# Performance work log

Hardware: AMD Instinct MI355X
Metric: run time of the kernel (lower is better)

## Reference

```python
import jax, jax.numpy as jnp
import numpy as np

DIMS = 256


def setup_inputs() -> dict:
    key = jax.random.key(0)
    ks = jax.random.split(key, 7)
    c = DIMS
    x = jax.random.normal(ks[0], (8, c, 64, 64), dtype=jnp.float32)
    s = 1.0 / np.sqrt(c)  # conv2d default init scale ~ U(-1/sqrt(fan_in),..)
    wq = jax.random.uniform(ks[1], (c, c), jnp.float32, -s, s)
    wk = jax.random.uniform(ks[2], (c, c), jnp.float32, -s, s)
    wv = jax.random.uniform(ks[3], (c, c), jnp.float32, -s, s)
    bq = jax.random.uniform(ks[4], (c,), jnp.float32, -s, s)
    bk = jax.random.uniform(ks[5], (c,), jnp.float32, -s, s)
    bv = jax.random.uniform(ks[6], (c,), jnp.float32, -s, s)
    return {"x": x, "wq": wq, "wk": wk, "wv": wv, "bq": bq, "bk": bk, "bv": bv}


def reference(x, wq, wk, wv, bq, bk, bv):
    b, c, h, w = x.shape
    xt = x.reshape(b, c, h * w).transpose(0, 2, 1)  # (b, hw, c)
    # 1x1 conv == per-pixel linear over channels; wq has shape (out_c, in_c)
    q = xt @ wq.T + bq  # (b, hw, c)
    k = xt @ wk.T + bk
    v = xt @ wv.T + bv
    scores = jnp.einsum('bnc,bmc->bnm', q, k) / jnp.sqrt(jnp.asarray(c, x.dtype))
    attn = jax.nn.softmax(scores, axis=-1)  # (b, hw, hw)
    out = jnp.einsum('bnm,bmc->bnc', attn, v)  # (b, hw, c)
    return out.transpose(0, 2, 1).reshape(b, c, h, w)
```

## Files before the change

kernel.cpp:

```cpp
#include <hip/hip_runtime.h>

#define NB 8
#define CC 256
#define NN 4096
#define KVB 64
#define NT (NN / KVB)

typedef __attribute__((ext_vector_type(8))) __bf16 bf16x8;
typedef __attribute__((ext_vector_type(4))) float f32x4;
typedef unsigned short u16;
typedef unsigned int u32;

#define GLL(g, l) __builtin_amdgcn_global_load_lds(                         \
    (const __attribute__((address_space(1))) void*)(g),                     \
    (__attribute__((address_space(3))) void*)(l), 16, 0, 0)

static __device__ __forceinline__ u16 f2b(float f) {
  unsigned u = __float_as_uint(f);
  u += 0x7FFF + ((u >> 16) & 1);
  return (u16)(u >> 16);
}

static __device__ __forceinline__ void plswap(u32& a, u32& b) {
  asm volatile("v_permlane32_swap_b32 %0, %1" : "+v"(a), "+v"(b));
}
static __device__ __forceinline__ void plswap16(u32& a, u32& b) {
  asm volatile("v_permlane16_swap_b32 %0, %1" : "+v"(a), "+v"(b));
}

__global__ __launch_bounds__(256) void k_cvtw(const float* __restrict__ wq,
                                              const float* __restrict__ wk,
                                              const float* __restrict__ wv,
                                              u16* __restrict__ wb) {
  const int i = blockIdx.x * 256 + threadIdx.x;
  const int z = blockIdx.y;
  const float* s = z == 0 ? wq : (z == 1 ? wk : wv);
  wb[(size_t)z * CC * CC + i] = f2b(s[i]);
}

__global__ __launch_bounds__(256) void k_qkv(const float* __restrict__ x,
                                             const u16* __restrict__ wb,
                                             const float* __restrict__ bq,
                                             const float* __restrict__ bk,
                                             const float* __restrict__ bv,
                                             u16* __restrict__ Qb,
                                             u16* __restrict__ Kb,
                                             u16* __restrict__ VTb) {
  __shared__ __align__(16) u16 At[64 * 256];

  const int b = blockIdx.y, n0 = blockIdx.x * 64;
  const int tid = threadIdx.x;
  const int wid = tid >> 6, lane = tid & 63;
  const int lr = lane & 15, lq = lane >> 4;

  {
    const int ccol = (lane & 15) * 4;
#pragma unroll
    for (int i = 0; i < 16; ++i) {
      const int c = wid * 64 + i * 4 + (lane >> 4);
      const f32x4 v = *(const f32x4*)(x + ((size_t)b * CC + c) * NN + n0 + ccol);
#pragma unroll
      for (int j = 0; j < 4; ++j) {
        const int nr = ccol + j;
        *(u16*)((char*)At + nr * 512 + ((c * 2) ^ ((nr & 7) << 4))) = f2b(v[j]);
      }
    }
  }
  __syncthreads();

  const int i0 = wid * 64;
#pragma unroll
  for (int z = 0; z < 3; ++z) {
    const u16* w = wb + (size_t)z * CC * CC;
    const float* bias = z == 0 ? bq : (z == 1 ? bk : bv);
    const float sc = z == 0 ? 0.09016844136959962f : 1.0f;

    f32x4 acc[4][4];
#pragma unroll
    for (int mt = 0; mt < 4; ++mt)
#pragma unroll
      for (int it = 0; it < 4; ++it) acc[mt][it] = (f32x4){0.f, 0.f, 0.f, 0.f};

#pragma unroll
    for (int s = 0; s < 8; ++s) {
      const int kb2 = s * 64 + lq * 16;
      bf16x8 av[4], bm[4];
#pragma unroll
      for (int mt = 0; mt < 4; ++mt) {
        const int row = mt * 16 + lr;
        av[mt] = *(const bf16x8*)((const char*)At + row * 512 + (kb2 ^ ((row & 7) << 4)));
      }
#pragma unroll
      for (int it = 0; it < 4; ++it)
        bm[it] = *(const bf16x8*)(w + (size_t)(i0 + it * 16 + lr) * CC + s * 32 + lq * 8);
#pragma unroll
      for (int mt = 0; mt < 4; ++mt)
#pragma unroll
        for (int it = 0; it < 4; ++it)
          acc[mt][it] = __builtin_amdgcn_mfma_f32_16x16x32_bf16(av[mt], bm[it], acc[mt][it], 0, 0, 0);
    }

#pragma unroll
    for (int it = 0; it < 4; ++it) {
      const int i = i0 + it * 16 + lr;
      const float bb = bias[i];
#pragma unroll
      for (int mt = 0; mt < 4; ++mt) {
        f32x4 v = acc[mt][it];
        if (z == 2) {
          ushort4 p;
          p.x = f2b(v[0] + bb);
          p.y = f2b(v[1] + bb);
          p.z = f2b(v[2] + bb);
          p.w = f2b(v[3] + bb);
          *(ushort4*)(VTb + ((size_t)b * CC + i) * NN + n0 + mt * 16 + lq * 4) = p;
        } else {
          u16* O = (z == 0 ? Qb : Kb) + ((size_t)b * NN + n0 + mt * 16 + lq * 4) * CC + i;
#pragma unroll
          for (int r = 0; r < 4; ++r) O[(size_t)r * CC] = f2b((v[r] + bb) * sc);
        }
      }
    }
  }
}

__global__ __launch_bounds__(512, 2) void k_attn(const u16* __restrict__ Qb,
                                                 const u16* __restrict__ Kb,
                                                 const u16* __restrict__ VTb,
                                                 float* __restrict__ out) {
  __shared__ __align__(16) char smem[131072];
  __shared__ float l_s[2][128];

  const int bid = blockIdx.x;
  const int b = bid & 7;
  const int q0 = (bid >> 3) * 128;
  const int tid = threadIdx.x;
  const int wid = tid >> 6, lane = tid & 63;
  const int lr = lane & 15, lq = lane >> 4;
  const int kvg = wid & 1, qg = wid >> 1;

  const char* Kbase = (const char*)(Kb + (size_t)b * NN * CC);
  const char* Vbase = (const char*)(VTb + (size_t)b * CC * NN);

  const int kc0 = wid * 4;
  const int krow_off = lane >> 5;
  const int kbyt = (lane & 31) * 16;
  const int vrow_off = lane >> 3;
  const int vbyt = (lane & 7) * 16;

  auto stage = [&](int buf, int kv) {
#pragma unroll
    for (int i = 0; i < 4; ++i) {
      const int c = kc0 + i;
      const int row = c * 2 + krow_off;
      GLL(Kbase + (size_t)(kv + row) * (CC * 2) + (kbyt ^ ((row & 7) << 4)),
          smem + buf * 32768 + c * 1024);
      const int vr = c * 8 + vrow_off;
      GLL(Vbase + (size_t)vr * (NN * 2) + (size_t)kv * 2 + (vbyt ^ ((vr & 7) << 4)),
          smem + 65536 + buf * 32768 + c * 1024);
    }
  };

  bf16x8 qf[16];
  {
    const u16* Qp = Qb + ((size_t)b * NN + q0 + qg * 32 + lr) * CC + lq * 8;
#pragma unroll
    for (int qt = 0; qt < 2; ++qt)
#pragma unroll
      for (int s = 0; s < 8; ++s)
        qf[qt * 8 + s] = *(const bf16x8*)(Qp + (size_t)qt * 16 * CC + s * 32);
  }

  f32x4 oacc[2][16];
#pragma unroll
  for (int qt = 0; qt < 2; ++qt)
#pragma unroll
    for (int ct = 0; ct < 16; ++ct) oacc[qt][ct] = (f32x4){0.f, 0.f, 0.f, 0.f};
  float lpart[2] = {0.f, 0.f};

  f32x4 sacc[2][2];
  auto qk = [&](int buf) {
#pragma unroll
    for (int kvt = 0; kvt < 2; ++kvt)
#pragma unroll
      for (int qt = 0; qt < 2; ++qt) sacc[kvt][qt] = (f32x4){0.f, 0.f, 0.f, 0.f};
    __builtin_amdgcn_s_setprio(1);
#pragma unroll
    for (int s = 0; s < 8; ++s) {
      const int cb = s * 64 + lq * 16;
#pragma unroll
      for (int kvt = 0; kvt < 2; ++kvt) {
        const int row = kvg * 32 + kvt * 16 + lr;
        const bf16x8 kf = *(const bf16x8*)(smem + buf * 32768 +
                                           row * 512 + (cb ^ ((row & 7) << 4)));
        sacc[kvt][0] = __builtin_amdgcn_mfma_f32_16x16x32_bf16(kf, qf[s], sacc[kvt][0], 0, 0, 0);
        sacc[kvt][1] = __builtin_amdgcn_mfma_f32_16x16x32_bf16(kf, qf[8 + s], sacc[kvt][1], 0, 0, 0);
      }
    }
    __builtin_amdgcn_s_setprio(0);
  };

  stage(0, 0);
  asm volatile("s_waitcnt vmcnt(0)" ::: "memory");
  __builtin_amdgcn_s_barrier();
  stage(1, KVB);
  qk(0);

  for (int t = 0; t < NT; ++t) {
    const int cur = t & 1;

    u32 w2q[2][4];
#pragma unroll
    for (int qt = 0; qt < 2; ++qt) {
#pragma unroll
      for (int kvt = 0; kvt < 2; ++kvt) {
        const float p0 = __builtin_amdgcn_exp2f(sacc[kvt][qt][0]);
        const float p1 = __builtin_amdgcn_exp2f(sacc[kvt][qt][1]);
        const float p2 = __builtin_amdgcn_exp2f(sacc[kvt][qt][2]);
        const float p3 = __builtin_amdgcn_exp2f(sacc[kvt][qt][3]);
        lpart[qt] += (p0 + p1) + (p2 + p3);
        const __bf16 b0 = (__bf16)p0, b1 = (__bf16)p1, b2 = (__bf16)p2, b3 = (__bf16)p3;
        w2q[qt][kvt * 2]     = (u32)__builtin_bit_cast(u16, b0) | ((u32)__builtin_bit_cast(u16, b1) << 16);
        w2q[qt][kvt * 2 + 1] = (u32)__builtin_bit_cast(u16, b2) | ((u32)__builtin_bit_cast(u16, b3) << 16);
      }
    }

    bf16x8 vfr[4];
#pragma unroll
    for (int ct = 0; ct < 4; ++ct) {
      const int row = ct * 16 + lr;
      vfr[ct] = *(const bf16x8*)(smem + 65536 + cur * 32768 + row * 128 +
                                 ((kvg * 64 + lq * 16) ^ ((row & 7) << 4)));
    }

    union { u32 u[4]; bf16x8 v; } pa[2];
#pragma unroll
    for (int qt = 0; qt < 2; ++qt) {
#pragma unroll
      for (int h = 0; h < 2; ++h) {
        u32 A = w2q[qt][h], B = w2q[qt][2 + h];
        plswap(A, B);
        plswap16(A, B);
        pa[qt].u[h] = A;
        pa[qt].u[2 + h] = B;
      }
    }

    __builtin_amdgcn_s_setprio(1);
#pragma unroll
    for (int ct = 0; ct < 16; ++ct) {
      const int row = ct * 16 + lr;
      const bf16x8 vf = (ct < 4) ? vfr[ct]
          : *(const bf16x8*)(smem + 65536 + cur * 32768 + row * 128 +
                             ((kvg * 64 + lq * 16) ^ ((row & 7) << 4)));
      oacc[0][ct] = __builtin_amdgcn_mfma_f32_16x16x32_bf16(pa[0].v, vf, oacc[0][ct], 0, 0, 0);
      oacc[1][ct] = __builtin_amdgcn_mfma_f32_16x16x32_bf16(pa[1].v, vf, oacc[1][ct], 0, 0, 0);
    }
    __builtin_amdgcn_s_setprio(0);

    asm volatile("" ::: "memory");
    asm volatile("s_waitcnt vmcnt(0)" ::: "memory");
    __builtin_amdgcn_s_barrier();

    if (t < NT - 1) {
      if (t < NT - 2) stage(cur, (t + 2) * KVB);
      qk(cur ^ 1);
    }
  }

#pragma unroll
  for (int qt = 0; qt < 2; ++qt) {
    lpart[qt] += __shfl_xor(lpart[qt], 16);
    lpart[qt] += __shfl_xor(lpart[qt], 32);
  }
  if (lq == 0) {
    l_s[kvg][qg * 32 + lr] = lpart[0];
    l_s[kvg][qg * 32 + 16 + lr] = lpart[1];
  }
  __syncthreads();

  float linv[2][4];
#pragma unroll
  for (int qt = 0; qt < 2; ++qt)
#pragma unroll
    for (int r = 0; r < 4; ++r) {
      const int idx = qg * 32 + qt * 16 + lq * 4 + r;
      linv[qt][r] = 1.f / (l_s[0][idx] + l_s[1][idx]);
    }

  if (kvg == 1) {
#pragma unroll
    for (int qt = 0; qt < 2; ++qt)
#pragma unroll
      for (int ct = 0; ct < 16; ++ct) {
        const int row = ct * 16 + lr;
        *(f32x4*)(smem + qg * 32768 + row * 128 +
                  ((qt * 64 + lq * 16) ^ ((row & 7) << 4))) = oacc[qt][ct];
      }
  }
  __syncthreads();
  if (kvg == 0) {
    float* op = out + (size_t)b * CC * NN;
#pragma unroll
    for (int qt = 0; qt < 2; ++qt)
#pragma unroll
      for (int ct = 0; ct < 16; ++ct) {
        const int row = ct * 16 + lr;
        const f32x4 o1 = *(const f32x4*)(smem + qg * 32768 + row * 128 +
                                         ((qt * 64 + lq * 16) ^ ((row & 7) << 4)));
        f32x4 v = {(oacc[qt][ct][0] + o1[0]) * linv[qt][0],
                   (oacc[qt][ct][1] + o1[1]) * linv[qt][1],
                   (oacc[qt][ct][2] + o1[2]) * linv[qt][2],
                   (oacc[qt][ct][3] + o1[3]) * linv[qt][3]};
        *(f32x4*)(op + (size_t)row * NN + q0 + qg * 32 + qt * 16 + lq * 4) = v;
      }
  }
}

extern "C" void kernel_launch(void* const* d_in, const int* in_sizes, int n_in,
                              void* d_out, int out_size, void* d_ws, size_t ws_size,
                              hipStream_t stream) {
  const float* x = (const float*)d_in[0];
  const float* wq = (const float*)d_in[1];
  const float* wk = (const float*)d_in[2];
  const float* wv = (const float*)d_in[3];
  const float* bq = (const float*)d_in[4];
  const float* bk = (const float*)d_in[5];
  const float* bv = (const float*)d_in[6];
  float* out = (float*)d_out;

  u16* Qb = (u16*)d_ws;
  u16* Kb = Qb + (size_t)NB * NN * CC;
  u16* VTb = Kb + (size_t)NB * NN * CC;
  u16* wb = VTb + (size_t)NB * NN * CC;

  k_cvtw<<<dim3(CC * CC / 256, 3), 256, 0, stream>>>(wq, wk, wv, wb);
  k_qkv<<<dim3(NN / 64, NB), 256, 0, stream>>>(x, wb, bq, bk, bv, Qb, Kb, VTb);
  k_attn<<<dim3(NN / 128 * NB), 512, 0, stream>>>(Qb, Kb, VTb, out);
}
```

Before: 206.9 us.

## Interleave QK of next tile with PV of current tile using triple-buffered V

Restructures the attention main loop so each iteration interleaves the QK^T MFMAs for tile t+1 with the PV MFMAs for tile t in a single instruction stream. This needs V kept for one more stage, so V gets a three-slot ring buffer and shared memory grows to 160KB. The aim is to overlap LDS reads, softmax exp work and MFMA issue across the two GEMMs. The larger shared-memory footprint may lower occupancy below the two blocks per CU that the launch bounds ask for.

```diff
diff --git a/kernel.cpp b/kernel.cpp
--- a/kernel.cpp
+++ b/kernel.cpp
@@ -128,8 +128,7 @@
                                                  const u16* __restrict__ Kb,
                                                  const u16* __restrict__ VTb,
                                                  float* __restrict__ out) {
-  __shared__ __align__(16) char smem[131072];
-  __shared__ float l_s[2][128];
+  __shared__ __align__(16) char smem[163840];
 
   const int bid = blockIdx.x;
   const int b = bid & 7;
@@ -148,16 +147,22 @@
   const int vrow_off = lane >> 3;
   const int vbyt = (lane & 7) * 16;
 
-  auto stage = [&](int buf, int kv) {
+  auto stageK = [&](int buf, int kv) {
 #pragma unroll
     for (int i = 0; i < 4; ++i) {
       const int c = kc0 + i;
       const int row = c * 2 + krow_off;
       GLL(Kbase + (size_t)(kv + row) * (CC * 2) + (kbyt ^ ((row & 7) << 4)),
           smem + buf * 32768 + c * 1024);
+    }
+  };
+  auto stageV = [&](int slot, int kv) {
+#pragma unroll
+    for (int i = 0; i < 4; ++i) {
+      const int c = kc0 + i;
       const int vr = c * 8 + vrow_off;
       GLL(Vbase + (size_t)vr * (NN * 2) + (size_t)kv * 2 + (vbyt ^ ((vr & 7) << 4)),
-          smem + 65536 + buf * 32768 + c * 1024);
+          smem + 65536 + slot * 32768 + c * 1024);
     }
   };
 
@@ -178,37 +183,10 @@
     for (int ct = 0; ct < 16; ++ct) oacc[qt][ct] = (f32x4){0.f, 0.f, 0.f, 0.f};
   float lpart[2] = {0.f, 0.f};
 
-  f32x4 sacc[2][2];
-  auto qk = [&](int buf) {
-#pragma unroll
-    for (int kvt = 0; kvt < 2; ++kvt)
-#pragma unroll
-      for (int qt = 0; qt < 2; ++qt) sacc[kvt][qt] = (f32x4){0.f, 0.f, 0.f, 0.f};
-    __builtin_amdgcn_s_setprio(1);
-#pragma unroll
-    for (int s = 0; s < 8; ++s) {
-      const int cb = s * 64 + lq * 16;
-#pragma unroll
-      for (int kvt = 0; kvt < 2; ++kvt) {
-        const int row = kvg * 32 + kvt * 16 + lr;
-        const bf16x8 kf = *(const bf16x8*)(smem + buf * 32768 +
-                                           row * 512 + (cb ^ ((row & 7) << 4)));
-        sacc[kvt][0] = __builtin_amdgcn_mfma_f32_16x16x32_bf16(kf, qf[s], sacc[kvt][0], 0, 0, 0);
-        sacc[kvt][1] = __builtin_amdgcn_mfma_f32_16x16x32_bf16(kf, qf[8 + s], sacc[kvt][1], 0, 0, 0);
-      }
-    }
-    __builtin_amdgcn_s_setprio(0);
-  };
-
-  stage(0, 0);
-  asm volatile("s_waitcnt vmcnt(0)" ::: "memory");
-  __builtin_amdgcn_s_barrier();
-  stage(1, KVB);
-  qk(0);
-
-  for (int t = 0; t < NT; ++t) {
-    const int cur = t & 1;
-
+  union PU { u32 u[4]; bf16x8 v; };
+  PU pa[2];
+
+  auto smblock = [&](f32x4 (&sacc)[2][2]) {
     u32 w2q[2][4];
 #pragma unroll
     for (int qt = 0; qt < 2; ++qt) {
@@ -224,16 +202,6 @@
         w2q[qt][kvt * 2 + 1] = (u32)__builtin_bit_cast(u16, b2) | ((u32)__builtin_bit_cast(u16, b3) << 16);
       }
     }
-
-    bf16x8 vfr[4];
-#pragma unroll
-    for (int ct = 0; ct < 4; ++ct) {
-      const int row = ct * 16 + lr;
-      vfr[ct] = *(const bf16x8*)(smem + 65536 + cur * 32768 + row * 128 +
-                                 ((kvg * 64 + lq * 16) ^ ((row & 7) << 4)));
-    }
-
-    union { u32 u[4]; bf16x8 v; } pa[2];
 #pragma unroll
     for (int qt = 0; qt < 2; ++qt) {
 #pragma unroll
@@ -245,37 +213,97 @@
         pa[qt].u[2 + h] = B;
       }
     }
-
+  };
+
+  stageK(0, 0); stageV(0, 0);
+  asm volatile("s_waitcnt vmcnt(0)" ::: "memory");
+  __builtin_amdgcn_s_barrier();
+  stageK(1, KVB); stageV(1, KVB);
+  {
+    f32x4 sacc[2][2];
+#pragma unroll
+    for (int kvt = 0; kvt < 2; ++kvt)
+#pragma unroll
+      for (int qt = 0; qt < 2; ++qt) sacc[kvt][qt] = (f32x4){0.f, 0.f, 0.f, 0.f};
     __builtin_amdgcn_s_setprio(1);
 #pragma unroll
-    for (int ct = 0; ct < 16; ++ct) {
-      const int row = ct * 16 + lr;
-      const bf16x8 vf = (ct < 4) ? vfr[ct]
-          : *(const bf16x8*)(smem + 65536 + cur * 32768 + row * 128 +
-                             ((kvg * 64 + lq * 16) ^ ((row & 7) << 4)));
-      oacc[0][ct] = __builtin_amdgcn_mfma_f32_16x16x32_bf16(pa[0].v, vf, oacc[0][ct], 0, 0, 0);
-      oacc[1][ct] = __builtin_amdgcn_mfma_f32_16x16x32_bf16(pa[1].v, vf, oacc[1][ct], 0, 0, 0);
+    for (int s = 0; s < 8; ++s) {
+      const int cb = s * 64 + lq * 16;
+#pragma unroll
+      for (int kvt = 0; kvt < 2; ++kvt) {
+        const int row = kvg * 32 + kvt * 16 + lr;
+        const bf16x8 kf = *(const bf16x8*)(smem + row * 512 + (cb ^ ((row & 7) << 4)));
+        sacc[kvt][0] = __builtin_amdgcn_mfma_f32_16x16x32_bf16(kf, qf[s], sacc[kvt][0], 0, 0, 0);
+        sacc[kvt][1] = __builtin_amdgcn_mfma_f32_16x16x32_bf16(kf, qf[8 + s], sacc[kvt][1], 0, 0, 0);
+      }
     }
     __builtin_amdgcn_s_setprio(0);
+    smblock(sacc);
+  }
+  asm volatile("s_waitcnt vmcnt(0)" ::: "memory");
+  __builtin_amdgcn_s_barrier();
+
+  for (int t = 0; t < NT - 1; ++t) {
+    const int kcur = t & 1;
+    const int vs = t % 3;
+    int vs2 = vs + 2; if (vs2 >= 3) vs2 -= 3;
+    if (t + 2 < NT) { stageK(kcur, (t + 2) * KVB); stageV(vs2, (t + 2) * KVB); }
+
+    f32x4 sacc[2][2];
+#pragma unroll
+    for (int kvt = 0; kvt < 2; ++kvt)
+#pragma unroll
+      for (int qt = 0; qt < 2; ++qt) sacc[kvt][qt] = (f32x4){0.f, 0.f, 0.f, 0.f};
+
+    const char* kb = smem + (kcur ^ 1) * 32768;
+    const char* vb = smem + 65536 + vs * 32768;
+    __builtin_amdgcn_s_setprio(1);
+#pragma unroll
+    for (int i = 0; i < 16; ++i) {
+      const int s = i >> 1, kvt = i & 1;
+      const int krow = kvg * 32 + kvt * 16 + lr;
+      const bf16x8 kf = *(const bf16x8*)(kb + krow * 512 +
+                                         ((s * 64 + lq * 16) ^ ((krow & 7) << 4)));
+      sacc[kvt][0] = __builtin_amdgcn_mfma_f32_16x16x32_bf16(kf, qf[s], sacc[kvt][0], 0, 0, 0);
+      sacc[kvt][1] = __builtin_amdgcn_mfma_f32_16x16x32_bf16(kf, qf[8 + s], sacc[kvt][1], 0, 0, 0);
+      const int vrow = i * 16 + lr;
+      const bf16x8 vf = *(const bf16x8*)(vb + vrow * 128 +
+                                         ((kvg * 64 + lq * 16) ^ ((vrow & 7) << 4)));
+      oacc[0][i] = __builtin_amdgcn_mfma_f32_16x16x32_bf16(pa[0].v, vf, oacc[0][i], 0, 0, 0);
+      oacc[1][i] = __builtin_amdgcn_mfma_f32_16x16x32_bf16(pa[1].v, vf, oacc[1][i], 0, 0, 0);
+    }
+    __builtin_amdgcn_s_setprio(0);
+
+    smblock(sacc);
 
     asm volatile("" ::: "memory");
     asm volatile("s_waitcnt vmcnt(0)" ::: "memory");
     __builtin_amdgcn_s_barrier();
-
-    if (t < NT - 1) {
-      if (t < NT - 2) stage(cur, (t + 2) * KVB);
-      qk(cur ^ 1);
-    }
-  }
-
+  }
+
+  {
+    const char* vb = smem + 65536 + ((NT - 1) % 3) * 32768;
+    __builtin_amdgcn_s_setprio(1);
+#pragma unroll
+    for (int i = 0; i < 16; ++i) {
+      const int vrow = i * 16 + lr;
+      const bf16x8 vf = *(const bf16x8*)(vb + vrow * 128 +
+                                         ((kvg * 64 + lq * 16) ^ ((vrow & 7) << 4)));
+      oacc[0][i] = __builtin_amdgcn_mfma_f32_16x16x32_bf16(pa[0].v, vf, oacc[0][i], 0, 0, 0);
+      oacc[1][i] = __builtin_amdgcn_mfma_f32_16x16x32_bf16(pa[1].v, vf, oacc[1][i], 0, 0, 0);
+    }
+    __builtin_amdgcn_s_setprio(0);
+  }
+
+  float* l_s = (float*)(smem + 131072);
 #pragma unroll
   for (int qt = 0; qt < 2; ++qt) {
     lpart[qt] += __shfl_xor(lpart[qt], 16);
     lpart[qt] += __shfl_xor(lpart[qt], 32);
   }
   if (lq == 0) {
-    l_s[kvg][qg * 32 + lr] = lpart[0];
-    l_s[kvg][qg * 32 + 16 + lr] = lpart[1];
+    l_s[kvg * 128 + qg * 32 + lr] = lpart[0];
+    l_s[kvg * 128 + qg * 32 + 16 + lr] = lpart[1];
   }
   __syncthreads();
 
@@ -285,7 +313,7 @@
 #pragma unroll
     for (int r = 0; r < 4; ++r) {
       const int idx = qg * 32 + qt * 16 + lq * 4 + r;
-      linv[qt][r] = 1.f / (l_s[0][idx] + l_s[1][idx]);
+      linv[qt][r] = 1.f / (l_s[idx] + l_s[128 + idx]);
     }
 
   if (kvg == 1) {
```

Measured after the change: 373.5 us. 1.81x slower.
